# Kernel tuning notes

Hardware: AMD Instinct MI355X
Metric: run time of the kernel (lower is better)

## Reference

```python
import jax, jax.numpy as jnp
import numpy as np

NPOINT = 2048
NSAMPLE = 32
BN_EPS = 1e-5


def fps(xyz_t, npoint):
    """Furthest point sampling. xyz_t: [B,N,3] -> idx [B,npoint] (starts at index 0)."""
    B, N, _ = xyz_t.shape

    def step(carry, _):
        dist, last = carry  # dist [B,N], last [B]
        centroid = jnp.take_along_axis(xyz_t, last[:, None, None], axis=1)  # [B,1,3]
        d = jnp.sum((xyz_t - centroid) ** 2, axis=-1)  # [B,N]
        dist = jnp.minimum(dist, d)
        nxt = jnp.argmax(dist, axis=1).astype(jnp.int32)
        return (dist, nxt), last

    init = (jnp.full((B, N), 1e10, xyz_t.dtype), jnp.zeros((B,), jnp.int32))
    _, idx = jax.lax.scan(step, init, None, length=npoint)  # [npoint,B]
    return jnp.transpose(idx)  # [B,npoint]


def knn(k, query_t, ref_t):
    """query_t [B,S,3], ref_t [B,N,3] -> k-nearest indices [B,S,k]."""
    d = (jnp.sum(query_t ** 2, -1)[:, :, None]
         + jnp.sum(ref_t ** 2, -1)[:, None, :]
         - 2.0 * jnp.einsum('bsc,bnc->bsn', query_t, ref_t))  # [B,S,N]
    _, idx = jax.lax.top_k(-d, k)
    return idx


def group(feat_t, idx):
    """feat_t [B,N,C], idx [B,S,K] -> [B,S,K,C] gathered neighbors."""
    return jax.vmap(lambda f, i: f[i])(feat_t, idx)


def setup_inputs():
    key = jax.random.key(0)
    ks = jax.random.split(key, 8)
    B, N, C, D = 8, 8192, 3, 3
    mlp = [32, 32, 64]
    inp = {
        'xyz': jax.random.normal(ks[0], (B, C, N), jnp.float32),
        'points': jax.random.normal(ks[1], (B, D, N), jnp.float32),
    }
    last = D + 3  # conv input channels = in_channel + 3
    for i, oc in enumerate(mlp):
        inp[f'w{i}'] = jax.random.normal(ks[2 + i], (oc, last), jnp.float32) * (1.0 / np.sqrt(last))
        inp[f'g{i}'] = jnp.ones((oc,), jnp.float32)
        inp[f'b{i}'] = jnp.zeros((oc,), jnp.float32)
        last = oc
    return inp


def reference(xyz, points, w0, g0, b0, w1, g1, b1, w2, g2, b2):
    xyz_t = jnp.transpose(xyz, (0, 2, 1))        # [B,N,3]
    points_t = jnp.transpose(points, (0, 2, 1))  # [B,N,D]

    fps_idx = fps(xyz_t, NPOINT)                             # [B,S]
    new_xyz_t = jax.vmap(lambda f, i: f[i])(xyz_t, fps_idx)  # [B,S,3]

    knn_idx = knn(NSAMPLE, new_xyz_t, xyz_t)                 # [B,S,K]
    grouped_xyz = group(xyz_t, knn_idx)                      # [B,S,K,3]
    pos_diff = grouped_xyz - new_xyz_t[:, :, None, :]        # [B,S,K,3]
    grouped_pts = group(points_t, knn_idx)                   # [B,S,K,D]

    x = jnp.concatenate([pos_diff, grouped_pts], axis=-1)    # [B,S,K,3+D]
    for w, g, b in ((w0, g0, b0), (w1, g1, b1), (w2, g2, b2)):
        x = jnp.einsum('oc,bskc->bsko', w, x)                # 1x1 conv, no bias
        mean = jnp.mean(x, axis=(0, 1, 2))                   # BatchNorm2d (training stats)
        var = jnp.var(x, axis=(0, 1, 2))
        x = jax.nn.relu(g * (x - mean) * jax.lax.rsqrt(var + BN_EPS) + b)

    new_points = jnp.max(x, axis=2)  # max over K neighbors -> [B,S,C']
    new_xyz = jnp.transpose(new_xyz_t, (0, 2, 1))      # [B,3,S]
    new_points = jnp.transpose(new_points, (0, 2, 1))  # [B,C',S]
    return (new_xyz, new_points, fps_idx)
```

## Files before the change

kernel.cpp:

```cpp
#include <hip/hip_runtime.h>
#include <hip/hip_bf16.h>
#include <math.h>


#define NB 8
#define NN 8192
#define NS 2048
#define NK 32

__global__ __launch_bounds__(256) void prep_kernel(const float* __restrict__ xyz,
                                                   const float* __restrict__ pts,
                                                   float4* __restrict__ xyz4,
                                                   float4* __restrict__ pts4) {
  int g = blockIdx.x * 256 + threadIdx.x;
  int b = g >> 13, n = g & 8191;
  const float* xb = xyz + b * 3 * NN;
  float x = xb[n], y = xb[NN + n], z = xb[2 * NN + n];
  xyz4[g] = make_float4(x, y, z, fmaf(x, x, fmaf(y, y, z * z)));
  const float* pb = pts + b * 3 * NN;
  pts4[g] = make_float4(pb[n], pb[NN + n], pb[2 * NN + n], 0.f);
}

template <int CTRL>
__device__ __forceinline__ float dpp_max(float v) {
  int o = __builtin_amdgcn_update_dpp(__float_as_int(v), __float_as_int(v),
                                      CTRL, 0xf, 0xf, false);
  return fmaxf(v, __int_as_float(o));
}

__global__ __launch_bounds__(256, 1) void fps_kernel(const float4* __restrict__ xyz4,
                                                     float* __restrict__ out_nxyz,
                                                     float* __restrict__ out_fps,
                                                     float4* __restrict__ nxyz4) {
  int b = blockIdx.x, tid = threadIdx.x;
  int lane = tid & 63, wid = tid >> 6;
  __shared__ unsigned long long wslot[2][4];
  const float4* xb = xyz4 + b * NN;

  float px[32], py[32], pz[32], dist[32];
#pragma unroll
  for (int j = 0; j < 32; ++j) {
    float4 t = xb[(tid << 5) + j];
    px[j] = t.x; py[j] = t.y; pz[j] = t.z;
    dist[j] = 1e10f;
  }
#pragma unroll
  for (int j = 0; j < 32; ++j) {
    asm volatile("" : "+v"(px[j]), "+v"(py[j]), "+v"(pz[j]));
  }

  float4 c0 = xb[0];
  float cx = c0.x, cy = c0.y, cz = c0.z;
  if (tid == 0) {
    nxyz4[b * NS] = c0;
    out_nxyz[b * 3 * NS] = c0.x;
    out_nxyz[b * 3 * NS + NS] = c0.y;
    out_nxyz[b * 3 * NS + 2 * NS] = c0.z;
    out_fps[b * NS] = 0.f;
  }

  for (int s = 1; s < NS; ++s) {
    float best = -1.0f;
    int bj = 0;
#pragma unroll
    for (int j = 0; j < 32; ++j) {
      float dx = __fsub_rn(px[j], cx);
      float dy = __fsub_rn(py[j], cy);
      float dz = __fsub_rn(pz[j], cz);
      float d = __fadd_rn(__fadd_rn(__fmul_rn(dx, dx), __fmul_rn(dy, dy)),
                          __fmul_rn(dz, dz));
      d = fminf(dist[j], d);
      dist[j] = d;
      bool gt = d > best;
      best = gt ? d : best;
      bj = gt ? j : bj;
    }

    float m = best;
    m = dpp_max<0x111>(m);
    m = dpp_max<0x112>(m);
    m = dpp_max<0x114>(m);
    m = dpp_max<0x118>(m);
    m = dpp_max<0x142>(m);
    m = dpp_max<0x143>(m);
    float wmax = __int_as_float(__builtin_amdgcn_readlane(__float_as_int(m), 63));

    unsigned long long bl = __ballot(best == wmax);
    int l0 = __ffsll((unsigned long long)bl) - 1;
    int gcand = (tid << 5) + bj;
    int gw = __builtin_amdgcn_readlane(gcand, l0);

    if (lane == 0)
      wslot[s & 1][wid] = (((unsigned long long)__float_as_uint(wmax)) << 32) |
                          (unsigned)(8191 - gw);
    __syncthreads();

    unsigned long long v0 = wslot[s & 1][0], v1 = wslot[s & 1][1];
    unsigned long long v2 = wslot[s & 1][2], v3 = wslot[s & 1][3];
    unsigned long long va = v0 > v1 ? v0 : v1;
    unsigned long long vb = v2 > v3 ? v2 : v3;
    unsigned long long vm = va > vb ? va : vb;
    int gid = 8191 - (int)(unsigned)(vm & 0xFFFFFFFFull);
    gid = __builtin_amdgcn_readfirstlane(gid);

    float4 c = xb[gid];
    cx = c.x; cy = c.y; cz = c.z;
    if (tid == 0) {
      nxyz4[b * NS + s] = c;
      out_nxyz[b * 3 * NS + s] = c.x;
      out_nxyz[b * 3 * NS + NS + s] = c.y;
      out_nxyz[b * 3 * NS + 2 * NS + s] = c.z;
      out_fps[b * NS + s] = (float)gid;
    }
  }
}

__device__ __forceinline__ void insert32(float (&a)[32], float f) {
#pragma unroll
  for (int i = 31; i >= 1; --i) a[i] = fminf(a[i], fmaxf(a[i - 1], f));
  a[0] = fminf(a[0], f);
}

__global__ __launch_bounds__(256) void knn_kernel(const float4* __restrict__ xyz4,
                                                  const float4* __restrict__ nxyz4,
                                                  int* __restrict__ knn) {
  __shared__ float lbuf[256][33];
  int b = blockIdx.x >> 5, tile = blockIdx.x & 31;
  int tid = threadIdx.x;
  int q = tid & 63, chunk = tid >> 6;
  float4 Q = nxyz4[b * NS + tile * 64 + q];
  float qq = Q.w;
  float mx = -2.f * Q.x, my = -2.f * Q.y, mz = -2.f * Q.z;
  float arr[32];
#pragma unroll
  for (int i = 0; i < 32; ++i) arr[i] = __uint_as_float(0x7f7fffffu);

  const float4* refs = xyz4 + b * NN + chunk * 2048;
  int rbase = chunk * 2048;
  for (int r = 0; r < 2048; ++r) {
    float4 R = refs[r];
    float d = fmaf(R.x, mx, fmaf(R.y, my, fmaf(R.z, mz, R.w + qq)));
    d = fmaxf(d, 0.f);
    float f = __uint_as_float((__float_as_uint(d) & 0xFFFFE000u) | (unsigned)(rbase + r));
    if (f < arr[31]) insert32(arr, f);
  }
#pragma unroll
  for (int i = 0; i < 32; ++i) lbuf[tid][i] = arr[i];
  __syncthreads();
  if (tid < 64) {
    for (int c = 1; c < 4; ++c)
      for (int i = 0; i < 32; ++i) {
        float f = lbuf[c * 64 + tid][i];
        if (f < arr[31]) insert32(arr, f);
      }
    int base = (b * NS + tile * 64 + tid) * NK;
#pragma unroll
    for (int i = 0; i < 32; ++i) knn[base + i] = (int)(__float_as_uint(arr[i]) & 0x1FFFu);
  }
}

template <int STAGE>
__global__ __launch_bounds__(256) void mlp_kernel(
    const float4* __restrict__ xyz4, const float4* __restrict__ pts4,
    const float4* __restrict__ nxyz4, const int* __restrict__ knn,
    const float* __restrict__ w0, const float* __restrict__ w1,
    const float* __restrict__ w2, const float* __restrict__ ab,
    float* __restrict__ partials, float* __restrict__ out_np) {
  constexpr int C = (STAGE == 2) ? 64 : 32;
  constexpr int SM = (STAGE == 3) ? 8 * 64 * 32 : 512;
  __shared__ float smem[SM];
  int blk = blockIdx.x;
  int b = blk >> 6, s0 = (blk & 63) * 32;
  int tid = threadIdx.x, sl = tid & 31, ksec = tid >> 5;
  int lane = tid & 63, wid = tid >> 6;
  int s = s0 + sl;
  float4 Q = nxyz4[b * NS + s];
  const float4* xb = xyz4 + b * NN;
  const float4* pb = pts4 + b * NN;
  const int* kb = knn + (b * NS + s) * NK + ksec * 4;

  float acc1[(STAGE == 3) ? 64 : C];
  float acc2[(STAGE == 3) ? 1 : C];
  if constexpr (STAGE == 3) {
#pragma unroll
    for (int o = 0; o < 64; ++o) acc1[o] = -3.4e38f;
  } else {
#pragma unroll
    for (int o = 0; o < C; ++o) { acc1[o] = 0.f; acc2[o] = 0.f; }
  }

  for (int kk = 0; kk < 4; ++kk) {
    int nid = kb[kk];
    float4 R = xb[nid];
    float4 P = pb[nid];
    float x0[6] = {R.x - Q.x, R.y - Q.y, R.z - Q.z, P.x, P.y, P.z};
    float h[32];
#pragma unroll
    for (int o = 0; o < 32; ++o) {
      float a = w0[o * 6] * x0[0];
#pragma unroll
      for (int c = 1; c < 6; ++c) a = fmaf(w0[o * 6 + c], x0[c], a);
      h[o] = a;
    }
    if constexpr (STAGE == 0) {
#pragma unroll
      for (int o = 0; o < 32; ++o) { acc1[o] += h[o]; acc2[o] = fmaf(h[o], h[o], acc2[o]); }
    } else {
#pragma unroll
      for (int o = 0; o < 32; ++o) h[o] = fmaxf(fmaf(h[o], ab[o], ab[64 + o]), 0.f);
      float h1[32];
#pragma unroll
      for (int o = 0; o < 32; ++o) {
        float a = 0.f;
#pragma unroll
        for (int i = 0; i < 32; ++i) a = fmaf(w1[o * 32 + i], h[i], a);
        h1[o] = a;
      }
      if constexpr (STAGE == 1) {
#pragma unroll
        for (int o = 0; o < 32; ++o) { acc1[o] += h1[o]; acc2[o] = fmaf(h1[o], h1[o], acc2[o]); }
      } else {
#pragma unroll
        for (int o = 0; o < 32; ++o) h1[o] = fmaxf(fmaf(h1[o], ab[128 + o], ab[192 + o]), 0.f);
#pragma unroll
        for (int o = 0; o < 64; ++o) {
          float a = 0.f;
#pragma unroll
          for (int i = 0; i < 32; ++i) a = fmaf(w2[o * 32 + i], h1[i], a);
          if constexpr (STAGE == 2) {
            acc1[o] += a;
            acc2[o] = fmaf(a, a, acc2[o]);
          } else {
            acc1[o] = fmaxf(acc1[o], fmaxf(fmaf(a, ab[256 + o], ab[320 + o]), 0.f));
          }
        }
      }
    }
  }

  if constexpr (STAGE < 3) {
#pragma unroll
    for (int o = 0; o < C; ++o) {
      float v1 = acc1[o], v2 = acc2[o];
#pragma unroll
      for (int d = 1; d < 64; d <<= 1) { v1 += __shfl_xor(v1, d); v2 += __shfl_xor(v2, d); }
      acc1[o] = v1; acc2[o] = v2;
    }
    if (lane == 0) {
#pragma unroll
      for (int o = 0; o < C; ++o) {
        smem[wid * 2 * C + o] = acc1[o];
        smem[wid * 2 * C + C + o] = acc2[o];
      }
    }
    __syncthreads();
    if (tid < 2 * C) {
      float v = smem[tid] + smem[2 * C + tid] + smem[4 * C + tid] + smem[6 * C + tid];
      partials[blk * 128 + tid] = v;
    }
  } else {
#pragma unroll
    for (int o = 0; o < 64; ++o) smem[ksec * 2048 + o * 32 + sl] = acc1[o];
    __syncthreads();
#pragma unroll
    for (int i = 0; i < 8; ++i) {
      int e = i * 256 + tid;
      int ch = e >> 5, ss = e & 31;
      float v = smem[ch * 32 + ss];
#pragma unroll
      for (int ks = 1; ks < 8; ++ks) v = fmaxf(v, smem[ks * 2048 + ch * 32 + ss]);
      out_np[b * 64 * NS + ch * NS + s0 + ss] = v;
    }
  }
}

__global__ __launch_bounds__(256) void finalize_kernel(const float* __restrict__ partials,
                                                       const float* __restrict__ g,
                                                       const float* __restrict__ bt,
                                                       float* __restrict__ ab, int C) {
  __shared__ float sm[256];
  int tid = threadIdx.x;
  int ch = tid & 127, half = tid >> 7;
  float acc = 0.f;
  if (ch < 2 * C) {
    const float* p = partials + half * 256 * 128 + ch;
    for (int i = 0; i < 256; ++i) acc += p[i * 128];
  }
  sm[half * 128 + ch] = acc;
  __syncthreads();
  if (tid < C) {
    float s1 = sm[tid] + sm[128 + tid];
    float s2 = sm[C + tid] + sm[128 + C + tid];
    const float ninv = 1.0f / 524288.0f;
    float mean = s1 * ninv;
    float var = s2 * ninv - mean * mean;
    float inv = 1.0f / sqrtf(var + 1e-5f);
    float a = g[tid] * inv;
    ab[tid] = a;
    ab[64 + tid] = bt[tid] - mean * a;
  }
}

extern "C" void kernel_launch(void* const* d_in, const int* in_sizes, int n_in,
                              void* d_out, int out_size, void* d_ws, size_t ws_size,
                              hipStream_t stream) {
  const float* xyz = (const float*)d_in[0];
  const float* pts = (const float*)d_in[1];
  const float* w0 = (const float*)d_in[2];
  const float* g0 = (const float*)d_in[3];
  const float* b0 = (const float*)d_in[4];
  const float* w1 = (const float*)d_in[5];
  const float* g1 = (const float*)d_in[6];
  const float* b1 = (const float*)d_in[7];
  const float* w2 = (const float*)d_in[8];
  const float* g2 = (const float*)d_in[9];
  const float* b2 = (const float*)d_in[10];
  float* out = (float*)d_out;
  float* ws = (float*)d_ws;

  float4* xyz4 = (float4*)ws;
  float4* pts4 = (float4*)(ws + 262144);
  float4* nxyz4 = (float4*)(ws + 524288);
  int* knn = (int*)(ws + 589824);
  float* partials = ws + 1114112;
  float* ab = ws + 1310720;
  float* out_np = out + 49152;
  float* out_fps = out + 1097728;

  prep_kernel<<<256, 256, 0, stream>>>(xyz, pts, xyz4, pts4);
  fps_kernel<<<NB, 256, 0, stream>>>(xyz4, out, out_fps, nxyz4);
  knn_kernel<<<256, 256, 0, stream>>>(xyz4, nxyz4, knn);

  mlp_kernel<0><<<512, 256, 0, stream>>>(xyz4, pts4, nxyz4, knn, w0, w1, w2, ab, partials, nullptr);
  finalize_kernel<<<1, 256, 0, stream>>>(partials, g0, b0, ab, 32);
  mlp_kernel<1><<<512, 256, 0, stream>>>(xyz4, pts4, nxyz4, knn, w0, w1, w2, ab, partials + 65536, nullptr);
  finalize_kernel<<<1, 256, 0, stream>>>(partials + 65536, g1, b1, ab + 128, 32);
  mlp_kernel<2><<<512, 256, 0, stream>>>(xyz4, pts4, nxyz4, knn, w0, w1, w2, ab, partials + 131072, nullptr);
  finalize_kernel<<<1, 256, 0, stream>>>(partials + 131072, g2, b2, ab + 256, 64);
  mlp_kernel<3><<<512, 256, 0, stream>>>(xyz4, pts4, nxyz4, knn, w0, w1, w2, ab, nullptr, out_np);
}
```

Measured before the change: 3.444 ms.

## Widen FPS to 512 threads with packed float2 math and LDS point table

The furthest-point-sampling kernel now runs with 512 threads, so each thread holds 16 points instead of 32, which halves the serial per-thread work in each of the 2048 dependent iterations. Distances are computed on two-wide float vectors to allow packed FP32 instructions. The argmax is split into a max reduction followed by an index search, instead of a compare-select chain carried through every step. The batch's points are also staged in LDS so that fetching the next centroid avoids a global load. In exchange, the cross-wave reduction now combines 8 slots instead of 4, and the kernel uses 128KB of LDS.

```diff
diff --git a/kernel.cpp b/kernel.cpp
--- a/kernel.cpp
+++ b/kernel.cpp
@@ -7,6 +7,8 @@
 #define NN 8192
 #define NS 2048
 #define NK 32
+
+typedef float f32x2 __attribute__((ext_vector_type(2)));
 
 __global__ __launch_bounds__(256) void prep_kernel(const float* __restrict__ xyz,
                                                    const float* __restrict__ pts,
@@ -28,25 +30,28 @@
   return fmaxf(v, __int_as_float(o));
 }
 
-__global__ __launch_bounds__(256, 1) void fps_kernel(const float4* __restrict__ xyz4,
+__global__ __launch_bounds__(512, 1) void fps_kernel(const float4* __restrict__ xyz4,
                                                      float* __restrict__ out_nxyz,
                                                      float* __restrict__ out_fps,
                                                      float4* __restrict__ nxyz4) {
+#pragma clang fp contract(off)
   int b = blockIdx.x, tid = threadIdx.x;
   int lane = tid & 63, wid = tid >> 6;
-  __shared__ unsigned long long wslot[2][4];
+  __shared__ float4 tbl[NN];
+  __shared__ unsigned long long kslot[2][8];
   const float4* xb = xyz4 + b * NN;
 
-  float px[32], py[32], pz[32], dist[32];
-#pragma unroll
-  for (int j = 0; j < 32; ++j) {
-    float4 t = xb[(tid << 5) + j];
-    px[j] = t.x; py[j] = t.y; pz[j] = t.z;
-    dist[j] = 1e10f;
-  }
-#pragma unroll
-  for (int j = 0; j < 32; ++j) {
-    asm volatile("" : "+v"(px[j]), "+v"(py[j]), "+v"(pz[j]));
+  f32x2 px[8], py[8], pz[8], dist[8];
+#pragma unroll
+  for (int jj = 0; jj < 8; ++jj) {
+    float4 t0 = xb[(tid << 4) + 2 * jj];
+    float4 t1 = xb[(tid << 4) + 2 * jj + 1];
+    tbl[(tid << 4) + 2 * jj] = t0;
+    tbl[(tid << 4) + 2 * jj + 1] = t1;
+    px[jj] = (f32x2){t0.x, t1.x};
+    py[jj] = (f32x2){t0.y, t1.y};
+    pz[jj] = (f32x2){t0.z, t1.z};
+    dist[jj] = (f32x2){1e10f, 1e10f};
   }
 
   float4 c0 = xb[0];
@@ -60,50 +65,62 @@
   }
 
   for (int s = 1; s < NS; ++s) {
-    float best = -1.0f;
+    f32x2 c2x = {cx, cx}, c2y = {cy, cy}, c2z = {cz, cz};
+#pragma unroll
+    for (int jj = 0; jj < 8; ++jj) {
+      f32x2 dx = px[jj] - c2x;
+      f32x2 dy = py[jj] - c2y;
+      f32x2 dz = pz[jj] - c2z;
+      f32x2 d = (dx * dx + dy * dy) + dz * dz;
+      f32x2 dm;
+      dm[0] = fminf(dist[jj][0], d[0]);
+      dm[1] = fminf(dist[jj][1], d[1]);
+      dist[jj] = dm;
+    }
+    f32x2 m2 = dist[0];
+#pragma unroll
+    for (int jj = 1; jj < 8; ++jj) {
+      m2[0] = fmaxf(m2[0], dist[jj][0]);
+      m2[1] = fmaxf(m2[1], dist[jj][1]);
+    }
+    float best = fmaxf(m2[0], m2[1]);
     int bj = 0;
 #pragma unroll
-    for (int j = 0; j < 32; ++j) {
-      float dx = __fsub_rn(px[j], cx);
-      float dy = __fsub_rn(py[j], cy);
-      float dz = __fsub_rn(pz[j], cz);
-      float d = __fadd_rn(__fadd_rn(__fmul_rn(dx, dx), __fmul_rn(dy, dy)),
-                          __fmul_rn(dz, dz));
-      d = fminf(dist[j], d);
-      dist[j] = d;
-      bool gt = d > best;
-      best = gt ? d : best;
-      bj = gt ? j : bj;
-    }
-
-    float m = best;
-    m = dpp_max<0x111>(m);
-    m = dpp_max<0x112>(m);
-    m = dpp_max<0x114>(m);
-    m = dpp_max<0x118>(m);
-    m = dpp_max<0x142>(m);
-    m = dpp_max<0x143>(m);
-    float wmax = __int_as_float(__builtin_amdgcn_readlane(__float_as_int(m), 63));
+    for (int j = 15; j >= 0; --j)
+      bj = (dist[j >> 1][j & 1] == best) ? j : bj;
+
+    float mm = best;
+    mm = dpp_max<0x111>(mm);
+    mm = dpp_max<0x112>(mm);
+    mm = dpp_max<0x114>(mm);
+    mm = dpp_max<0x118>(mm);
+    mm = dpp_max<0x142>(mm);
+    mm = dpp_max<0x143>(mm);
+    float wmax = __int_as_float(__builtin_amdgcn_readlane(__float_as_int(mm), 63));
 
     unsigned long long bl = __ballot(best == wmax);
-    int l0 = __ffsll((unsigned long long)bl) - 1;
-    int gcand = (tid << 5) + bj;
-    int gw = __builtin_amdgcn_readlane(gcand, l0);
+    int l0 = __ffsll(bl) - 1;
+    int gw = __builtin_amdgcn_readlane((tid << 4) + bj, l0);
 
     if (lane == 0)
-      wslot[s & 1][wid] = (((unsigned long long)__float_as_uint(wmax)) << 32) |
+      kslot[s & 1][wid] = (((unsigned long long)__float_as_uint(wmax)) << 32) |
                           (unsigned)(8191 - gw);
     __syncthreads();
 
-    unsigned long long v0 = wslot[s & 1][0], v1 = wslot[s & 1][1];
-    unsigned long long v2 = wslot[s & 1][2], v3 = wslot[s & 1][3];
-    unsigned long long va = v0 > v1 ? v0 : v1;
-    unsigned long long vb = v2 > v3 ? v2 : v3;
-    unsigned long long vm = va > vb ? va : vb;
-    int gid = 8191 - (int)(unsigned)(vm & 0xFFFFFFFFull);
+    const unsigned long long* ks = kslot[s & 1];
+    unsigned long long k0 = ks[0], k1 = ks[1], k2 = ks[2], k3 = ks[3];
+    unsigned long long k4 = ks[4], k5 = ks[5], k6 = ks[6], k7 = ks[7];
+    unsigned long long a0 = k0 > k1 ? k0 : k1;
+    unsigned long long a1 = k2 > k3 ? k2 : k3;
+    unsigned long long a2 = k4 > k5 ? k4 : k5;
+    unsigned long long a3 = k6 > k7 ? k6 : k7;
+    unsigned long long b0 = a0 > a1 ? a0 : a1;
+    unsigned long long b1 = a2 > a3 ? a2 : a3;
+    unsigned long long km = b0 > b1 ? b0 : b1;
+    int gid = 8191 - (int)((unsigned)km & 0x1FFFu);
     gid = __builtin_amdgcn_readfirstlane(gid);
 
-    float4 c = xb[gid];
+    float4 c = tbl[gid];
     cx = c.x; cy = c.y; cz = c.z;
     if (tid == 0) {
       nxyz4[b * NS + s] = c;
@@ -328,7 +345,7 @@
   float* out_fps = out + 1097728;
 
   prep_kernel<<<256, 256, 0, stream>>>(xyz, pts, xyz4, pts4);
-  fps_kernel<<<NB, 256, 0, stream>>>(xyz4, out, out_fps, nxyz4);
+  fps_kernel<<<NB, 512, 0, stream>>>(xyz4, out, out_fps, nxyz4);
   knn_kernel<<<256, 256, 0, stream>>>(xyz4, nxyz4, knn);
 
   mlp_kernel<0><<<512, 256, 0, stream>>>(xyz4, pts4, nxyz4, knn, w0, w1, w2, ab, partials, nullptr);
```

New measurement: 2.928 ms. 15.0% less time.
